# Optimization experiments

Hardware: AMD Instinct MI355X
Metric: run time of the kernel (lower is better)

Reference implementation:

```python
import jax, jax.numpy as jnp
import numpy as np

LAYER_NUMBER = 1  # coeff for query_key_layer_scaling; cancels mathematically
HEAD_DIM = 128

def setup_inputs() -> dict:
    key = jax.random.key(0)
    k1, k2, k3, k4 = jax.random.split(key, 4)
    s, b, h, d = 2048, 2, 16, HEAD_DIM
    return {
        "query_layer": jax.random.normal(k1, (s, b, h, d), dtype=jnp.float32),
        "key_layer": jax.random.normal(k2, (s, b, h, d), dtype=jnp.float32),
        "value_layer": jax.random.normal(k3, (s, b, h, d), dtype=jnp.float32),
        "attention_mask": jax.random.randint(k4, (b, 1, s, s), 0, 2).astype(jnp.bool_),
    }

def reference(query_layer, key_layer, value_layer, attention_mask):
    s, b, h, d = query_layer.shape
    # norm_factor = sqrt(d) * layer_number; softmax scale (coeff) = layer_number
    norm_factor = jnp.sqrt(jnp.asarray(d, jnp.float32)) * LAYER_NUMBER
    coeff = jnp.asarray(LAYER_NUMBER, jnp.float32)
    # raw scores [b, h, sq, sk]
    scores = jnp.einsum('sbhd,tbhd->bhst', query_layer, key_layer) / norm_factor
    # fused scale-mask-softmax, in fp32 (attention_softmax_in_fp32=True)
    scores32 = scores.astype(jnp.float32) * coeff
    scores32 = jnp.where(attention_mask, jnp.float32(-10000.0), scores32)
    probs = jax.nn.softmax(scores32, axis=-1).astype(query_layer.dtype)
    # dropout p=0.0 -> identity
    # context: [b, h, sq, d] -> [sq, b, h*d]
    ctx = jnp.einsum('bhst,tbhd->sbhd', probs, value_layer)
    return ctx.reshape(s, b, h * d)
```

## Files before the change

kernel.cpp:

```cpp
#include <hip/hip_runtime.h>
#include <hip/hip_bf16.h>

#define S_LEN 2048
#define NB 2
#define NH 16
#define DH 128
#define ROW_STRIDE (NB * NH * DH)
#define M_TILE 128
#define N_TILE 64
#define NKT (S_LEN / N_TILE)
#define NWORDS (NB * S_LEN * (S_LEN / 64))

typedef __bf16 bf16x8_t __attribute__((ext_vector_type(8)));
typedef __bf16 bf16x4_t __attribute__((ext_vector_type(4)));
typedef float  f32x4_t  __attribute__((ext_vector_type(4)));

#define LDS_KS 136
#define LDS_VS 72
#define LDS_PS 68

#if defined(__has_builtin)
#if __has_builtin(__builtin_amdgcn_exp2f)
#define EXP2F __builtin_amdgcn_exp2f
#else
#define EXP2F exp2f
#endif
#else
#define EXP2F exp2f
#endif

template <int CTRL>
__device__ __forceinline__ float dppmov(float x) {
    return __builtin_bit_cast(float,
        __builtin_amdgcn_update_dpp(0, __builtin_bit_cast(int, x), CTRL, 0xF, 0xF, true));
}
__device__ __forceinline__ float rowmax16(float x) {
    x = fmaxf(x, dppmov<0xB1>(x));
    x = fmaxf(x, dppmov<0x4E>(x));
    x = fmaxf(x, dppmov<0x141>(x));
    x = fmaxf(x, dppmov<0x140>(x));
    return x;
}
__device__ __forceinline__ float rowsum16(float x) {
    x += dppmov<0xB1>(x);
    x += dppmov<0x4E>(x);
    x += dppmov<0x141>(x);
    x += dppmov<0x140>(x);
    return x;
}

__global__ __launch_bounds__(256) void mask_pack(
    const int* __restrict__ Mg, unsigned long long* __restrict__ Wg)
{
    const int lane = threadIdx.x & 63;
    const int wv = (blockIdx.x * blockDim.x + threadIdx.x) >> 6;
#pragma unroll
    for (int i = 0; i < 4; ++i) {
        const int wid = wv * 4 + i;
        const int v = Mg[(size_t)wid * 64 + lane];
        const unsigned long long bal = __ballot(v != 0);
        if (lane == 0) Wg[wid] = bal;
    }
}

__global__ __launch_bounds__(256, 2) void fa_kernel(
    const float* __restrict__ Qg, const float* __restrict__ Kg,
    const float* __restrict__ Vg, const unsigned long long* __restrict__ Mw,
    float* __restrict__ Og)
{
    __shared__ __bf16 kT[64 * LDS_KS];
    __shared__ __bf16 vT[DH * LDS_VS];
    __shared__ __bf16 pT[4 * 32 * LDS_PS];

    const int tid  = threadIdx.x;
    const int wave = tid >> 6;
    const int lane = tid & 63;
    const int l15  = lane & 15;
    const int quad = lane >> 4;

    const int bid = blockIdx.x;
    const int qt  = bid & 15;
    const int bh  = bid >> 4;
    const int h   = bh & (NH - 1);
    const int b   = bh >> 4;

    const int q0       = qt * M_TILE;
    const int head_off = b * (NH * DH) + h * DH;

    const float kScale   = 1.44269504088896340736f / 11.31370849898476039f;
    const float kMaskVal = -14426.950408889634f;
    const float kThr     = 8.0f;

    const uint2* mrow = (const uint2*)Mw
        + (size_t)b * (S_LEN * (S_LEN / 64))
        + (size_t)(q0 + wave * 32) * (S_LEN / 64);

    bf16x8_t qf[2][4];
#pragma unroll
    for (int mt = 0; mt < 2; ++mt) {
        const int srow = q0 + wave * 32 + mt * 16 + l15;
        const float* qp = Qg + (size_t)srow * ROW_STRIDE + head_off + quad * 8;
#pragma unroll
        for (int kc = 0; kc < 4; ++kc) {
            float4 f0 = *(const float4*)(qp + kc * 32);
            float4 f1 = *(const float4*)(qp + kc * 32 + 4);
            bf16x8_t v;
            v[0] = (__bf16)f0.x; v[1] = (__bf16)f0.y;
            v[2] = (__bf16)f0.z; v[3] = (__bf16)f0.w;
            v[4] = (__bf16)f1.x; v[5] = (__bf16)f1.y;
            v[6] = (__bf16)f1.z; v[7] = (__bf16)f1.w;
            qf[mt][kc] = v;
        }
    }

    f32x4_t oacc[2][8];
    float mstate[2][4], lstate[2][4];
#pragma unroll
    for (int mt = 0; mt < 2; ++mt) {
#pragma unroll
        for (int dt = 0; dt < 8; ++dt) oacc[mt][dt] = {0.0f, 0.0f, 0.0f, 0.0f};
#pragma unroll
        for (int r = 0; r < 4; ++r) { mstate[mt][r] = -3.0e38f; lstate[mt][r] = 0.0f; }
    }

    __bf16* pW = &pT[wave * 32 * LDS_PS];

    for (int kt = 0; kt < NKT; ++kt) {
        const int t0 = kt * N_TILE;
        __syncthreads();

        {
            const int r0 = tid >> 5;
            const int c4 = (tid & 31) * 4;
            const float* kp = Kg + (size_t)(t0 + r0) * ROW_STRIDE + head_off + c4;
            __bf16* kd = &kT[r0 * LDS_KS + c4];
#pragma unroll
            for (int rr = 0; rr < 8; ++rr) {
                float4 f = *(const float4*)kp;
                bf16x4_t w;
                w[0] = (__bf16)f.x; w[1] = (__bf16)f.y;
                w[2] = (__bf16)f.z; w[3] = (__bf16)f.w;
                *(bf16x4_t*)kd = w;
                kp += 8 * ROW_STRIDE;
                kd += 8 * LDS_KS;
            }
        }
        {
            const int dv = tid & 31;
            const int tg = tid >> 5;
            const float* vbase = Vg + (size_t)(t0 + tg * 8) * ROW_STRIDE + head_off + dv;
#pragma unroll
            for (int j = 0; j < 4; ++j) {
                const int d = dv + j * 32;
#pragma unroll
                for (int tt = 0; tt < 2; ++tt) {
                    const float* vp = vbase + j * 32 + (size_t)(tt * 4) * ROW_STRIDE;
                    bf16x4_t w;
                    w[0] = (__bf16)vp[0 * ROW_STRIDE];
                    w[1] = (__bf16)vp[1 * ROW_STRIDE];
                    w[2] = (__bf16)vp[2 * ROW_STRIDE];
                    w[3] = (__bf16)vp[3 * ROW_STRIDE];
                    *(bf16x4_t*)&vT[d * LDS_VS + tg * 8 + tt * 4] = w;
                }
            }
        }
        __syncthreads();

        uint2 mw[2][4];
#pragma unroll
        for (int mt = 0; mt < 2; ++mt)
#pragma unroll
            for (int r = 0; r < 4; ++r)
                mw[mt][r] = mrow[(size_t)(mt * 16 + quad * 4 + r) * (S_LEN / 64) + kt];

        f32x4_t sacc[2][4];
#pragma unroll
        for (int mt = 0; mt < 2; ++mt)
#pragma unroll
            for (int n = 0; n < 4; ++n) sacc[mt][n] = {0.0f, 0.0f, 0.0f, 0.0f};
#pragma unroll
        for (int n = 0; n < 4; ++n) {
#pragma unroll
            for (int kc = 0; kc < 4; ++kc) {
                bf16x8_t kb = *(const bf16x8_t*)&kT[(n * 16 + l15) * LDS_KS + kc * 32 + quad * 8];
                sacc[0][n] = __builtin_amdgcn_mfma_f32_16x16x32_bf16(qf[0][kc], kb, sacc[0][n], 0, 0, 0);
                sacc[1][n] = __builtin_amdgcn_mfma_f32_16x16x32_bf16(qf[1][kc], kb, sacc[1][n], 0, 0, 0);
            }
        }

#pragma unroll
        for (int mt = 0; mt < 2; ++mt) {
            float sv[4][4];
            float tmv[4];
#pragma unroll
            for (int r = 0; r < 4; ++r) {
                const unsigned a0 = mw[mt][r].x >> l15;
                const unsigned a1 = mw[mt][r].y >> l15;
                sv[0][r] = (a0 & 1u)       ? kMaskVal : sacc[mt][0][r] * kScale;
                sv[1][r] = (a0 & 0x10000u) ? kMaskVal : sacc[mt][1][r] * kScale;
                sv[2][r] = (a1 & 1u)       ? kMaskVal : sacc[mt][2][r] * kScale;
                sv[3][r] = (a1 & 0x10000u) ? kMaskVal : sacc[mt][3][r] * kScale;
                float tm = fmaxf(fmaxf(sv[0][r], sv[1][r]), fmaxf(sv[2][r], sv[3][r]));
                tmv[r] = rowmax16(tm);
            }
            bool need = (tmv[0] > mstate[mt][0] + kThr) |
                        (tmv[1] > mstate[mt][1] + kThr) |
                        (tmv[2] > mstate[mt][2] + kThr) |
                        (tmv[3] > mstate[mt][3] + kThr);
            if (__any(need)) {
#pragma unroll
                for (int r = 0; r < 4; ++r) {
                    const float mold  = mstate[mt][r];
                    const float mnew  = fmaxf(mold, tmv[r]);
                    const float alpha = EXP2F(mold - mnew);
                    float rsum = 0.0f;
#pragma unroll
                    for (int n = 0; n < 4; ++n) {
                        float p = EXP2F(sv[n][r] - mnew);
                        rsum += p;
                        pW[(mt * 16 + quad * 4 + r) * LDS_PS + n * 16 + l15] = (__bf16)p;
                    }
                    rsum = rowsum16(rsum);
                    lstate[mt][r] = lstate[mt][r] * alpha + rsum;
                    mstate[mt][r] = mnew;
#pragma unroll
                    for (int dt = 0; dt < 8; ++dt) oacc[mt][dt][r] *= alpha;
                }
            } else {
#pragma unroll
                for (int r = 0; r < 4; ++r) {
                    const float mold = mstate[mt][r];
                    float rsum = 0.0f;
#pragma unroll
                    for (int n = 0; n < 4; ++n) {
                        float p = EXP2F(sv[n][r] - mold);
                        rsum += p;
                        pW[(mt * 16 + quad * 4 + r) * LDS_PS + n * 16 + l15] = (__bf16)p;
                    }
                    lstate[mt][r] += rowsum16(rsum);
                }
            }
        }

#pragma unroll
        for (int kc2 = 0; kc2 < 2; ++kc2) {
            bf16x8_t af[2];
#pragma unroll
            for (int mt = 0; mt < 2; ++mt) {
                bf16x4_t lo = *(const bf16x4_t*)&pW[(mt * 16 + l15) * LDS_PS + kc2 * 32 + quad * 8];
                bf16x4_t hi = *(const bf16x4_t*)&pW[(mt * 16 + l15) * LDS_PS + kc2 * 32 + quad * 8 + 4];
                af[mt] = __builtin_shufflevector(lo, hi, 0, 1, 2, 3, 4, 5, 6, 7);
            }
#pragma unroll
            for (int dt = 0; dt < 8; ++dt) {
                bf16x8_t bfr = *(const bf16x8_t*)&vT[(dt * 16 + l15) * LDS_VS + kc2 * 32 + quad * 8];
                oacc[0][dt] = __builtin_amdgcn_mfma_f32_16x16x32_bf16(af[0], bfr, oacc[0][dt], 0, 0, 0);
                oacc[1][dt] = __builtin_amdgcn_mfma_f32_16x16x32_bf16(af[1], bfr, oacc[1][dt], 0, 0, 0);
            }
        }
    }

#pragma unroll
    for (int mt = 0; mt < 2; ++mt) {
#pragma unroll
        for (int r = 0; r < 4; ++r) {
            const float inv = 1.0f / lstate[mt][r];
            const int srow = q0 + wave * 32 + mt * 16 + quad * 4 + r;
            float* op = Og + (size_t)srow * ROW_STRIDE + head_off + l15;
#pragma unroll
            for (int dt = 0; dt < 8; ++dt) op[dt * 16] = oacc[mt][dt][r] * inv;
        }
    }
}

extern "C" void kernel_launch(void* const* d_in, const int* in_sizes, int n_in,
                              void* d_out, int out_size, void* d_ws, size_t ws_size,
                              hipStream_t stream) {
    (void)in_sizes; (void)n_in; (void)ws_size; (void)out_size;
    const float* Q = (const float*)d_in[0];
    const float* K = (const float*)d_in[1];
    const float* V = (const float*)d_in[2];
    const int*   M = (const int*)d_in[3];
    float* O = (float*)d_out;
    unsigned long long* Mw = (unsigned long long*)d_ws;

    dim3 pgrid(NWORDS / 4 * 64 / 256);
    hipLaunchKernelGGL(mask_pack, pgrid, dim3(256), 0, stream, M, Mw);

    dim3 grid(NB * NH * (S_LEN / M_TILE));
    dim3 block(256);
    hipLaunchKernelGGL(fa_kernel, grid, block, 0, stream, Q, K, V, Mw, O);
}
```

Baseline: 301.2 us.

## Pre-convert K/V to bf16 and double-buffer tiles via direct global-to-LDS loads

Adds a prep kernel that converts K to bf16 in per-head contiguous layout, transposes V to bf16, and packs the mask in the same launch. The attention kernel then stages K/V tiles into swizzled, double-buffered LDS using global_load_lds, prefetching the next tile while computing the current one. This removes repeated fp32 loads and conversions of K/V from every query tile and overlaps memory with MFMA work. The cost is a larger workspace, an extra pass over K/V, and a fallback path kept for when the workspace is too small.

```diff
diff --git a/kernel.cpp b/kernel.cpp
--- a/kernel.cpp
+++ b/kernel.cpp
@@ -15,9 +15,8 @@
 typedef __bf16 bf16x4_t __attribute__((ext_vector_type(4)));
 typedef float  f32x4_t  __attribute__((ext_vector_type(4)));
 
-#define LDS_KS 136
-#define LDS_VS 72
-#define LDS_PS 68
+#define AS1 __attribute__((address_space(1)))
+#define AS3 __attribute__((address_space(3)))
 
 #if defined(__has_builtin)
 #if __has_builtin(__builtin_amdgcn_exp2f)
@@ -29,6 +28,10 @@
 #define EXP2F exp2f
 #endif
 
+__device__ __forceinline__ void gload_lds16(const void* g, void* l) {
+    __builtin_amdgcn_global_load_lds((const AS1 void*)g, (AS3 void*)l, 16, 0, 0);
+}
+
 template <int CTRL>
 __device__ __forceinline__ float dppmov(float x) {
     return __builtin_bit_cast(float,
@@ -49,6 +52,71 @@
     return x;
 }
 
+__global__ __launch_bounds__(256) void prep_kernel(
+    const float* __restrict__ Kg, const float* __restrict__ Vg,
+    const int* __restrict__ Mg,
+    __bf16* __restrict__ Kb, __bf16* __restrict__ Vb,
+    unsigned long long* __restrict__ Wg)
+{
+    __shared__ float tf[64][129];
+    const int tid = threadIdx.x;
+    const int blk = blockIdx.x;
+
+    if (blk < 4096) {
+        const int idx = blk * 256 + tid;
+        const int d8 = (idx & 15) * 8;
+        const int t  = (idx >> 4) & (S_LEN - 1);
+        const int bh = idx >> 15;
+        const int b = bh >> 4, h = bh & (NH - 1);
+        const float* src = Kg + (size_t)t * ROW_STRIDE + b * (NH * DH) + h * DH + d8;
+        float4 f0 = *(const float4*)src;
+        float4 f1 = *(const float4*)(src + 4);
+        bf16x8_t v;
+        v[0] = (__bf16)f0.x; v[1] = (__bf16)f0.y; v[2] = (__bf16)f0.z; v[3] = (__bf16)f0.w;
+        v[4] = (__bf16)f1.x; v[5] = (__bf16)f1.y; v[6] = (__bf16)f1.z; v[7] = (__bf16)f1.w;
+        *(bf16x8_t*)(Kb + ((size_t)bh * S_LEN + t) * DH + d8) = v;
+    } else if (blk < 5120) {
+        const int vb = blk - 4096;
+        const int bh = vb >> 5;
+        const int tc = vb & 31;
+        const int b = bh >> 4, h = bh & (NH - 1);
+        const int t0 = tc * 64;
+        const int head_off = b * (NH * DH) + h * DH;
+#pragma unroll
+        for (int i = 0; i < 8; ++i) {
+            int idx = i * 256 + tid;
+            int t  = idx >> 5;
+            int d4 = (idx & 31) * 4;
+            float4 f = *(const float4*)(Vg + (size_t)(t0 + t) * ROW_STRIDE + head_off + d4);
+            tf[t][d4 + 0] = f.x; tf[t][d4 + 1] = f.y;
+            tf[t][d4 + 2] = f.z; tf[t][d4 + 3] = f.w;
+        }
+        __syncthreads();
+#pragma unroll
+        for (int i = 0; i < 8; ++i) {
+            int idx = i * 256 + tid;
+            int d  = idx >> 4;
+            int t4 = (idx & 15) * 4;
+            bf16x4_t w;
+            w[0] = (__bf16)tf[t4 + 0][d];
+            w[1] = (__bf16)tf[t4 + 1][d];
+            w[2] = (__bf16)tf[t4 + 2][d];
+            w[3] = (__bf16)tf[t4 + 3][d];
+            *(bf16x4_t*)(Vb + ((size_t)bh * DH + d) * S_LEN + t0 + t4) = w;
+        }
+    } else {
+        const int lane = tid & 63;
+        const int wv = ((blk - 5120) * 256 + tid) >> 6;
+#pragma unroll
+        for (int i = 0; i < 16; ++i) {
+            const int wid = wv * 16 + i;
+            const int v = Mg[(size_t)wid * 64 + lane];
+            const unsigned long long bal = __ballot(v != 0);
+            if (lane == 0) Wg[wid] = bal;
+        }
+    }
+}
+
 __global__ __launch_bounds__(256) void mask_pack(
     const int* __restrict__ Mg, unsigned long long* __restrict__ Wg)
 {
@@ -64,19 +132,20 @@
 }
 
 __global__ __launch_bounds__(256, 2) void fa_kernel(
-    const float* __restrict__ Qg, const float* __restrict__ Kg,
-    const float* __restrict__ Vg, const unsigned long long* __restrict__ Mw,
+    const float* __restrict__ Qg, const __bf16* __restrict__ Kb,
+    const __bf16* __restrict__ Vb, const unsigned long long* __restrict__ Mw,
     float* __restrict__ Og)
 {
-    __shared__ __bf16 kT[64 * LDS_KS];
-    __shared__ __bf16 vT[DH * LDS_VS];
-    __shared__ __bf16 pT[4 * 32 * LDS_PS];
+    __shared__ __bf16 kT[2][64 * 128];
+    __shared__ __bf16 vT[2][128 * 64];
+    __shared__ __bf16 pT[4 * 32 * 64];
 
     const int tid  = threadIdx.x;
     const int wave = tid >> 6;
     const int lane = tid & 63;
     const int l15  = lane & 15;
     const int quad = lane >> 4;
+    const int swz  = (l15 & 7) << 4;
 
     const int bid = blockIdx.x;
     const int qt  = bid & 15;
@@ -94,6 +163,21 @@
     const uint2* mrow = (const uint2*)Mw
         + (size_t)b * (S_LEN * (S_LEN / 64))
         + (size_t)(q0 + wave * 32) * (S_LEN / 64);
+
+    const char* KbBH = (const char*)(Kb + (size_t)bh * S_LEN * DH);
+    const char* VbBH = (const char*)(Vb + (size_t)bh * DH * S_LEN);
+
+    int kOff[4], vOff[4];
+#pragma unroll
+    for (int i = 0; i < 4; ++i) {
+        const int chunk = (wave * 4 + i) * 64 + lane;
+        const int tr = chunk >> 4;
+        const int ck = chunk & 15;
+        kOff[i] = tr * 256 + ((ck * 16) ^ ((tr & 7) << 4));
+        const int dv = chunk >> 3;
+        const int cv = chunk & 7;
+        vOff[i] = dv * (S_LEN * 2) + ((cv * 16) ^ ((dv & 7) << 4));
+    }
 
     bf16x8_t qf[2][4];
 #pragma unroll
@@ -123,6 +207,212 @@
         for (int r = 0; r < 4; ++r) { mstate[mt][r] = -3.0e38f; lstate[mt][r] = 0.0f; }
     }
 
+    char* pW = (char*)&pT[wave * 32 * 64];
+
+    auto STAGE = [&](int buf, int kt_) {
+        const char* ks = KbBH + (size_t)kt_ * (N_TILE * DH * 2);
+        const char* vs = VbBH + (size_t)kt_ * (N_TILE * 2);
+#pragma unroll
+        for (int i = 0; i < 4; ++i)
+            gload_lds16(ks + kOff[i], (char*)&kT[buf][0] + (wave * 4 + i) * 1024);
+#pragma unroll
+        for (int i = 0; i < 4; ++i)
+            gload_lds16(vs + vOff[i], (char*)&vT[buf][0] + (wave * 4 + i) * 1024);
+    };
+
+    STAGE(0, 0);
+    asm volatile("s_waitcnt vmcnt(0)" ::: "memory");
+    __builtin_amdgcn_s_barrier();
+    int cur = 0;
+
+    for (int kt = 0; kt < NKT; ++kt) {
+        if (kt + 1 < NKT) STAGE(cur ^ 1, kt + 1);
+
+        uint2 mw[2][4];
+#pragma unroll
+        for (int mt = 0; mt < 2; ++mt)
+#pragma unroll
+            for (int r = 0; r < 4; ++r)
+                mw[mt][r] = mrow[(size_t)(mt * 16 + quad * 4 + r) * (S_LEN / 64) + kt];
+
+        const char* kbuf = (const char*)&kT[cur][0];
+        f32x4_t sacc[2][4];
+#pragma unroll
+        for (int mt = 0; mt < 2; ++mt)
+#pragma unroll
+            for (int n = 0; n < 4; ++n) sacc[mt][n] = {0.0f, 0.0f, 0.0f, 0.0f};
+        __builtin_amdgcn_s_setprio(1);
+#pragma unroll
+        for (int n = 0; n < 4; ++n) {
+#pragma unroll
+            for (int kc = 0; kc < 4; ++kc) {
+                bf16x8_t kb = *(const bf16x8_t*)(kbuf + (n * 16 + l15) * 256
+                                                 + ((kc * 64 + quad * 16) ^ swz));
+                sacc[0][n] = __builtin_amdgcn_mfma_f32_16x16x32_bf16(qf[0][kc], kb, sacc[0][n], 0, 0, 0);
+                sacc[1][n] = __builtin_amdgcn_mfma_f32_16x16x32_bf16(qf[1][kc], kb, sacc[1][n], 0, 0, 0);
+            }
+        }
+        __builtin_amdgcn_s_setprio(0);
+
+#pragma unroll
+        for (int mt = 0; mt < 2; ++mt) {
+            float sv[4][4];
+            float tmv[4];
+#pragma unroll
+            for (int r = 0; r < 4; ++r) {
+                const unsigned a0 = mw[mt][r].x >> l15;
+                const unsigned a1 = mw[mt][r].y >> l15;
+                sv[0][r] = (a0 & 1u)       ? kMaskVal : sacc[mt][0][r] * kScale;
+                sv[1][r] = (a0 & 0x10000u) ? kMaskVal : sacc[mt][1][r] * kScale;
+                sv[2][r] = (a1 & 1u)       ? kMaskVal : sacc[mt][2][r] * kScale;
+                sv[3][r] = (a1 & 0x10000u) ? kMaskVal : sacc[mt][3][r] * kScale;
+                float tm = fmaxf(fmaxf(sv[0][r], sv[1][r]), fmaxf(sv[2][r], sv[3][r]));
+                tmv[r] = rowmax16(tm);
+            }
+            bool need = (tmv[0] > mstate[mt][0] + kThr) |
+                        (tmv[1] > mstate[mt][1] + kThr) |
+                        (tmv[2] > mstate[mt][2] + kThr) |
+                        (tmv[3] > mstate[mt][3] + kThr);
+            if (__any(need)) {
+#pragma unroll
+                for (int r = 0; r < 4; ++r) {
+                    const int prow = mt * 16 + quad * 4 + r;
+                    const int prswz = (prow & 7) << 4;
+                    const float mold  = mstate[mt][r];
+                    const float mnew  = fmaxf(mold, tmv[r]);
+                    const float alpha = EXP2F(mold - mnew);
+                    float rsum = 0.0f;
+#pragma unroll
+                    for (int n = 0; n < 4; ++n) {
+                        float p = EXP2F(sv[n][r] - mnew);
+                        rsum += p;
+                        *(__bf16*)(pW + prow * 128 + ((2 * (n * 16 + l15)) ^ prswz)) = (__bf16)p;
+                    }
+                    rsum = rowsum16(rsum);
+                    lstate[mt][r] = lstate[mt][r] * alpha + rsum;
+                    mstate[mt][r] = mnew;
+#pragma unroll
+                    for (int dt = 0; dt < 8; ++dt) oacc[mt][dt][r] *= alpha;
+                }
+            } else {
+#pragma unroll
+                for (int r = 0; r < 4; ++r) {
+                    const int prow = mt * 16 + quad * 4 + r;
+                    const int prswz = (prow & 7) << 4;
+                    const float mold = mstate[mt][r];
+                    float rsum = 0.0f;
+#pragma unroll
+                    for (int n = 0; n < 4; ++n) {
+                        float p = EXP2F(sv[n][r] - mold);
+                        rsum += p;
+                        *(__bf16*)(pW + prow * 128 + ((2 * (n * 16 + l15)) ^ prswz)) = (__bf16)p;
+                    }
+                    lstate[mt][r] += rowsum16(rsum);
+                }
+            }
+        }
+
+        const char* vbuf = (const char*)&vT[cur][0];
+        __builtin_amdgcn_s_setprio(1);
+#pragma unroll
+        for (int kc2 = 0; kc2 < 2; ++kc2) {
+            bf16x8_t af[2];
+#pragma unroll
+            for (int mt = 0; mt < 2; ++mt)
+                af[mt] = *(const bf16x8_t*)(pW + (mt * 16 + l15) * 128
+                                            + ((kc2 * 64 + quad * 16) ^ swz));
+#pragma unroll
+            for (int dt = 0; dt < 8; ++dt) {
+                bf16x8_t bfr = *(const bf16x8_t*)(vbuf + (dt * 16 + l15) * 128
+                                                  + ((kc2 * 64 + quad * 16) ^ swz));
+                oacc[0][dt] = __builtin_amdgcn_mfma_f32_16x16x32_bf16(af[0], bfr, oacc[0][dt], 0, 0, 0);
+                oacc[1][dt] = __builtin_amdgcn_mfma_f32_16x16x32_bf16(af[1], bfr, oacc[1][dt], 0, 0, 0);
+            }
+        }
+        __builtin_amdgcn_s_setprio(0);
+
+        asm volatile("s_waitcnt vmcnt(0)" ::: "memory");
+        __builtin_amdgcn_s_barrier();
+        cur ^= 1;
+    }
+
+#pragma unroll
+    for (int mt = 0; mt < 2; ++mt) {
+#pragma unroll
+        for (int r = 0; r < 4; ++r) {
+            const float inv = 1.0f / lstate[mt][r];
+            const int srow = q0 + wave * 32 + mt * 16 + quad * 4 + r;
+            float* op = Og + (size_t)srow * ROW_STRIDE + head_off + l15;
+#pragma unroll
+            for (int dt = 0; dt < 8; ++dt) op[dt * 16] = oacc[mt][dt][r] * inv;
+        }
+    }
+}
+
+#define LDS_KS 136
+#define LDS_VS 72
+#define LDS_PS 68
+
+__global__ __launch_bounds__(256, 2) void fa_kernel_fb(
+    const float* __restrict__ Qg, const float* __restrict__ Kg,
+    const float* __restrict__ Vg, const unsigned long long* __restrict__ Mw,
+    float* __restrict__ Og)
+{
+    __shared__ __bf16 kT[64 * LDS_KS];
+    __shared__ __bf16 vT[DH * LDS_VS];
+    __shared__ __bf16 pT[4 * 32 * LDS_PS];
+
+    const int tid  = threadIdx.x;
+    const int wave = tid >> 6;
+    const int lane = tid & 63;
+    const int l15  = lane & 15;
+    const int quad = lane >> 4;
+
+    const int bid = blockIdx.x;
+    const int qt  = bid & 15;
+    const int bh  = bid >> 4;
+    const int h   = bh & (NH - 1);
+    const int b   = bh >> 4;
+
+    const int q0       = qt * M_TILE;
+    const int head_off = b * (NH * DH) + h * DH;
+
+    const float kScale   = 1.44269504088896340736f / 11.31370849898476039f;
+    const float kMaskVal = -14426.950408889634f;
+    const float kThr     = 8.0f;
+
+    const uint2* mrow = (const uint2*)Mw
+        + (size_t)b * (S_LEN * (S_LEN / 64))
+        + (size_t)(q0 + wave * 32) * (S_LEN / 64);
+
+    bf16x8_t qf[2][4];
+#pragma unroll
+    for (int mt = 0; mt < 2; ++mt) {
+        const int srow = q0 + wave * 32 + mt * 16 + l15;
+        const float* qp = Qg + (size_t)srow * ROW_STRIDE + head_off + quad * 8;
+#pragma unroll
+        for (int kc = 0; kc < 4; ++kc) {
+            float4 f0 = *(const float4*)(qp + kc * 32);
+            float4 f1 = *(const float4*)(qp + kc * 32 + 4);
+            bf16x8_t v;
+            v[0] = (__bf16)f0.x; v[1] = (__bf16)f0.y;
+            v[2] = (__bf16)f0.z; v[3] = (__bf16)f0.w;
+            v[4] = (__bf16)f1.x; v[5] = (__bf16)f1.y;
+            v[6] = (__bf16)f1.z; v[7] = (__bf16)f1.w;
+            qf[mt][kc] = v;
+        }
+    }
+
+    f32x4_t oacc[2][8];
+    float mstate[2][4], lstate[2][4];
+#pragma unroll
+    for (int mt = 0; mt < 2; ++mt) {
+#pragma unroll
+        for (int dt = 0; dt < 8; ++dt) oacc[mt][dt] = {0.0f, 0.0f, 0.0f, 0.0f};
+#pragma unroll
+        for (int r = 0; r < 4; ++r) { mstate[mt][r] = -3.0e38f; lstate[mt][r] = 0.0f; }
+    }
+
     __bf16* pW = &pT[wave * 32 * LDS_PS];
 
     for (int kt = 0; kt < NKT; ++kt) {
@@ -276,18 +566,26 @@
 extern "C" void kernel_launch(void* const* d_in, const int* in_sizes, int n_in,
                               void* d_out, int out_size, void* d_ws, size_t ws_size,
                               hipStream_t stream) {
-    (void)in_sizes; (void)n_in; (void)ws_size; (void)out_size;
+    (void)in_sizes; (void)n_in; (void)out_size;
     const float* Q = (const float*)d_in[0];
     const float* K = (const float*)d_in[1];
     const float* V = (const float*)d_in[2];
     const int*   M = (const int*)d_in[3];
     float* O = (float*)d_out;
-    unsigned long long* Mw = (unsigned long long*)d_ws;
-
-    dim3 pgrid(NWORDS / 4 * 64 / 256);
-    hipLaunchKernelGGL(mask_pack, pgrid, dim3(256), 0, stream, M, Mw);
-
-    dim3 grid(NB * NH * (S_LEN / M_TILE));
-    dim3 block(256);
-    hipLaunchKernelGGL(fa_kernel, grid, block, 0, stream, Q, K, V, Mw, O);
-}
+
+    const size_t need_fast = ((size_t)33 << 20);
+
+    if (ws_size >= need_fast) {
+        __bf16* Kb = (__bf16*)d_ws;
+        __bf16* Vb = (__bf16*)((char*)d_ws + ((size_t)16 << 20));
+        unsigned long long* Mw = (unsigned long long*)((char*)d_ws + ((size_t)32 << 20));
+        hipLaunchKernelGGL(prep_kernel, dim3(7168), dim3(256), 0, stream, K, V, M, Kb, Vb, Mw);
+        hipLaunchKernelGGL(fa_kernel, dim3(NB * NH * (S_LEN / M_TILE)), dim3(256), 0, stream,
+                           Q, Kb, Vb, Mw, O);
+    } else {
+        unsigned long long* Mw = (unsigned long long*)d_ws;
+        hipLaunchKernelGGL(mask_pack, dim3(NWORDS / 4 * 64 / 256), dim3(256), 0, stream, M, Mw);
+        hipLaunchKernelGGL(fa_kernel_fb, dim3(NB * NH * (S_LEN / M_TILE)), dim3(256), 0, stream,
+                           Q, K, V, Mw, O);
+    }
+}
```

After: 296.9 us. No clear change (-1.4%).
